# Performance work log

Measured on AMD Instinct MI355X. Metric: run time of the kernel, lower is better.

## Reference

```python
import jax, jax.numpy as jnp
from jax import lax
import numpy as np

D_MODEL = 1024
D_STATE = 128
D_CONV = 4
EXPAND = 2
HEADDIM = 64
CHUNK = 10
D_INNER = EXPAND * D_MODEL          # 2048
NHEADS = D_INNER // HEADDIM         # 32
CONV_DIM = D_INNER + 2 * D_STATE    # 2304
BATCH, SEQ = 2, 1000


def setup_inputs() -> dict:
    key = jax.random.key(0)
    ks = jax.random.split(key, 9)
    n = lambda k, shp, sc: jax.random.normal(k, shp, dtype=jnp.float32) * sc
    return {
        "x": n(ks[0], (BATCH, SEQ, D_MODEL), 1.0),
        "W_in": n(ks[1], (2 * D_INNER + 2 * D_STATE + NHEADS, D_MODEL), 0.02),
        "conv_w": n(ks[2], (CONV_DIM, D_CONV), 0.2),
        "conv_b": n(ks[3], (CONV_DIM,), 0.02),
        "dt_bias": n(ks[4], (NHEADS,), 0.5),
        "A_log": jnp.log(jnp.linspace(1.0, 16.0, NHEADS)).astype(jnp.float32),
        "D": n(ks[6], (NHEADS,), 1.0),
        "norm_w": jnp.ones((D_INNER,), jnp.float32),
        "W_out": n(ks[8], (D_MODEL, D_INNER), 0.02),
    }


def segsum(x):
    # x: (..., T) -> (..., T, T) with out[i,j] = sum_{k=j+1..i} x_k for i>=j else -inf
    cs = jnp.cumsum(x, axis=-1)
    seg = cs[..., :, None] - cs[..., None, :]
    T = x.shape[-1]
    mask = jnp.tril(jnp.ones((T, T), bool))
    return jnp.where(mask, seg, -jnp.inf)


def ssd(x, A, Bm, Cm, chunk):
    # x: (b,l,h,p)  A: (b,l,h)  Bm,Cm: (b,l,n)  (ngroups=1, group dim squeezed)
    b, l, h, p = x.shape
    n = Bm.shape[-1]
    c = l // chunk
    xr = x.reshape(b, c, chunk, h, p)
    Ar = A.reshape(b, c, chunk, h).transpose(0, 3, 1, 2)      # (b,h,c,s)
    Br = Bm.reshape(b, c, chunk, n)
    Cr = Cm.reshape(b, c, chunk, n)
    Acs = jnp.cumsum(Ar, axis=-1)                              # (b,h,c,s)
    L = jnp.exp(segsum(Ar))                                    # (b,h,c,s,s)
    # intra-chunk (diagonal blocks)
    Y_diag = jnp.einsum('bcln,bcsn,bhcls,bcshp->bclhp', Cr, Br, L, xr)
    # per-chunk end states
    decay_states = jnp.exp(Acs[..., -1:] - Acs)                # (b,h,c,s)
    states = jnp.einsum('bcln,bhcl,bclhp->bchpn', Br, decay_states, xr)
    states = jnp.concatenate([jnp.zeros((b, 1, h, p, n), x.dtype), states], axis=1)
    # inter-chunk recurrence (parallel form)
    chunk_sums = jnp.pad(Acs[..., -1], ((0, 0), (0, 0), (1, 0)))  # (b,h,c+1)
    decay_chunk = jnp.exp(segsum(chunk_sums))                    # (b,h,c+1,c+1)
    new_states = jnp.einsum('bhzc,bchpn->bzhpn', decay_chunk, states)
    prev_states = new_states[:, :-1]                             # (b,c,h,p,n)
    # state -> output contribution
    Y_off = jnp.einsum('bcln,bchpn,bhcl->bclhp', Cr, prev_states, jnp.exp(Acs))
    return (Y_diag + Y_off).reshape(b, l, h, p)


def reference(x, W_in, conv_w, conv_b, dt_bias, A_log, D, norm_w, W_out):
    b, l, _ = x.shape
    zxbcdt = x @ W_in.T                                          # (b,l,4384)
    z = zxbcdt[..., :D_INNER]
    xBC = zxbcdt[..., D_INNER:D_INNER + CONV_DIM]
    dt = zxbcdt[..., D_INNER + CONV_DIM:]
    dt = jax.nn.softplus(dt + dt_bias)                           # (b,l,h)
    # causal depthwise conv1d
    xc = jnp.pad(xBC, ((0, 0), (D_CONV - 1, 0), (0, 0)))
    conv = lax.conv_general_dilated(
        xc.transpose(0, 2, 1), conv_w[:, None, :], (1,), 'VALID',
        feature_group_count=CONV_DIM,
        dimension_numbers=('NCH', 'OIH', 'NCH'))
    xBC = jax.nn.silu(conv.transpose(0, 2, 1) + conv_b)          # (b,l,conv_dim)
    x_ssm = xBC[..., :D_INNER].reshape(b, l, NHEADS, HEADDIM)
    Bm = xBC[..., D_INNER:D_INNER + D_STATE]
    Cm = xBC[..., D_INNER + D_STATE:]
    A = -jnp.exp(A_log)                                          # (h,)
    y = ssd(x_ssm * dt[..., None], A * dt, Bm, Cm, CHUNK)
    y = y + x_ssm * D[None, None, :, None]
    y = y.reshape(b, l, D_INNER)
    # gated RMSNorm
    y = y * jax.nn.silu(z)
    y = y * lax.rsqrt(jnp.mean(y * y, axis=-1, keepdims=True) + 1e-5) * norm_w
    return y @ W_out.T
```

## Files before the change

kernel.cpp:

```cpp
#include <hip/hip_runtime.h>
#include <hip/hip_bf16.h>

#define BATCHN 2
#define SEQL 1000
#define DMODEL 1024
#define DSTATE 128
#define HEADDIM 64
#define DINNER 2048
#define NHEADS 32
#define CONVDIM 2304
#define NPROJ 4384
#define TOKENS 2000
#define MPAD 2048
#define NPAD1 4608
#define QC 64
#define NCH 16

typedef __bf16 bfx8 __attribute__((ext_vector_type(8)));
typedef float fx4 __attribute__((ext_vector_type(4)));
typedef unsigned short u16x8 __attribute__((ext_vector_type(8)));

__device__ __forceinline__ unsigned short f2bf(float f) {
    unsigned int u = __builtin_bit_cast(unsigned int, f);
    u += 0x7FFFu + ((u >> 16) & 1u);
    return (unsigned short)(u >> 16);
}
__device__ __forceinline__ float bf2f(unsigned short u) {
    return __builtin_bit_cast(float, ((unsigned int)u) << 16);
}

__device__ __forceinline__ void gload16(const void* g, void* l) {
    __builtin_amdgcn_global_load_lds(
        (const __attribute__((address_space(1))) void*)g,
        (__attribute__((address_space(3))) void*)l, 16, 0, 0);
}

__global__ __launch_bounds__(256) void k_f2bf_pad(const float* __restrict__ src,
                                                  unsigned short* __restrict__ dst,
                                                  int n4src, int n4dst) {
    int i = blockIdx.x * 256 + threadIdx.x;
    if (i >= n4dst) return;
    ushort4 o = {0, 0, 0, 0};
    if (i < n4src) {
        float4 v = ((const float4*)src)[i];
        o.x = f2bf(v.x); o.y = f2bf(v.y); o.z = f2bf(v.z); o.w = f2bf(v.w);
    }
    ((ushort4*)dst)[i] = o;
}

__global__ __launch_bounds__(256) void k_dt(const float* __restrict__ x,
                                            const float* __restrict__ win,
                                            const float* __restrict__ dt_bias,
                                            float* __restrict__ dtv) {
    __shared__ float sx[8][1024];
    int t = threadIdx.x;
    int tok0 = blockIdx.x * 8;
    for (int i = t; i < 8 * 256; i += 256) {
        int tok = i >> 8, k4 = i & 255;
        ((float4*)&sx[tok][0])[k4] = ((const float4*)(x + (size_t)(tok0 + tok) * DMODEL))[k4];
    }
    __syncthreads();
    int tl = t >> 5, h = t & 31;
    const float4* wr_ = (const float4*)(win + (size_t)(2 * DINNER + 2 * DSTATE + h) * DMODEL);
    const float4* xr = (const float4*)&sx[tl][0];
    float acc = 0.f;
    #pragma unroll 4
    for (int k = 0; k < 256; ++k) {
        float4 a = xr[k], b = wr_[k];
        acc += a.x * b.x + a.y * b.y + a.z * b.z + a.w * b.w;
    }
    float v = acc + dt_bias[h];
    dtv[(size_t)(tok0 + tl) * NHEADS + h] = fmaxf(v, 0.f) + log1pf(expf(-fabsf(v)));
}

__global__ __launch_bounds__(512) void k_gemm256(const unsigned short* __restrict__ A,
                                                 const unsigned short* __restrict__ B,
                                                 float* __restrict__ C,
                                                 int Mstore, int N, int K,
                                                 int kc, size_t pstride) {
    __shared__ __attribute__((aligned(16))) unsigned short As[2][4096];
    __shared__ __attribute__((aligned(16))) unsigned short Bs[2][8192];
    int t = threadIdx.x;
    int lane = t & 63, wave = t >> 6;
    int wr = wave >> 2, wc = wave & 3;
    int m0 = blockIdx.y * 128, n0 = blockIdx.x * 256;
    int k0 = blockIdx.z * kc;
    int swcol = (((t & 3) ^ ((t >> 3) & 3)) * 8);
    const unsigned short* Ag  = A + (size_t)(m0 + (t >> 2)) * K + k0 + swcol;
    const unsigned short* Bg0 = B + (size_t)(n0 + (t >> 2)) * K + k0 + swcol;
    const unsigned short* Bg1 = Bg0 + (size_t)128 * K;
    gload16(Ag, &As[0][t * 8]);
    gload16(Bg0, &Bs[0][t * 8]);
    gload16(Bg1, &Bs[0][4096 + t * 8]);
    fx4 acc[4][4] = {};
    int fr = lane & 15, ks = lane >> 4;
    int sl = (ks ^ ((fr >> 1) & 3)) << 3;
    __syncthreads();
    int cur = 0;
    for (int kk = 32; kk < kc; kk += 32) {
        gload16(Ag + kk, &As[cur ^ 1][t * 8]);
        gload16(Bg0 + kk, &Bs[cur ^ 1][t * 8]);
        gload16(Bg1 + kk, &Bs[cur ^ 1][4096 + t * 8]);
        bfx8 a[4], b[4];
        #pragma unroll
        for (int m = 0; m < 4; ++m)
            a[m] = *(const bfx8*)&As[cur][(wr * 64 + m * 16 + fr) * 32 + sl];
        #pragma unroll
        for (int n = 0; n < 4; ++n)
            b[n] = *(const bfx8*)&Bs[cur][(wc * 64 + n * 16 + fr) * 32 + sl];
        #pragma unroll
        for (int m = 0; m < 4; ++m)
            #pragma unroll
            for (int n = 0; n < 4; ++n)
                acc[m][n] = __builtin_amdgcn_mfma_f32_16x16x32_bf16(a[m], b[n], acc[m][n], 0, 0, 0);
        __syncthreads();
        cur ^= 1;
    }
    {
        bfx8 a[4], b[4];
        #pragma unroll
        for (int m = 0; m < 4; ++m)
            a[m] = *(const bfx8*)&As[cur][(wr * 64 + m * 16 + fr) * 32 + sl];
        #pragma unroll
        for (int n = 0; n < 4; ++n)
            b[n] = *(const bfx8*)&Bs[cur][(wc * 64 + n * 16 + fr) * 32 + sl];
        #pragma unroll
        for (int m = 0; m < 4; ++m)
            #pragma unroll
            for (int n = 0; n < 4; ++n)
                acc[m][n] = __builtin_amdgcn_mfma_f32_16x16x32_bf16(a[m], b[n], acc[m][n], 0, 0, 0);
    }
    float* Cz = C + (size_t)blockIdx.z * pstride;
    #pragma unroll
    for (int m = 0; m < 4; ++m) {
        int rbase = m0 + wr * 64 + m * 16 + (lane >> 4) * 4;
        #pragma unroll
        for (int i = 0; i < 4; ++i) {
            int r = rbase + i;
            if (r < Mstore) {
                #pragma unroll
                for (int n = 0; n < 4; ++n) {
                    int c = n0 + wc * 64 + n * 16 + fr;
                    if (c < N) Cz[(size_t)r * N + c] = acc[m][n][i];
                }
            }
        }
    }
}

__global__ __launch_bounds__(256) void k_red(const float* __restrict__ part,
                                             float* __restrict__ out, int n4, size_t pstride4) {
    int i = blockIdx.x * 256 + threadIdx.x;
    if (i >= n4) return;
    const float4* p = (const float4*)part;
    float4 v0 = p[i];
    float4 v1 = p[i + pstride4];
    float4 v2 = p[i + 2 * pstride4];
    float4 v3 = p[i + 3 * pstride4];
    float4 o;
    o.x = (v0.x + v1.x) + (v2.x + v3.x);
    o.y = (v0.y + v1.y) + (v2.y + v3.y);
    o.z = (v0.z + v1.z) + (v2.z + v3.z);
    o.w = (v0.w + v1.w) + (v2.w + v3.w);
    ((float4*)out)[i] = o;
}

__global__ __launch_bounds__(256) void k_conv(const float* __restrict__ zx,
                                              const float* __restrict__ cw,
                                              const float* __restrict__ cb,
                                              float* __restrict__ xbc) {
    int idx = blockIdx.x * 256 + threadIdx.x;
    if (idx >= TOKENS * CONVDIM) return;
    int row = idx / CONVDIM;
    int col = idx - row * CONVDIM;
    int l = row % SEQL;
    float acc = cb[col];
    #pragma unroll
    for (int j = 0; j < 4; ++j) {
        int lj = l - 3 + j;
        if (lj >= 0)
            acc += zx[(size_t)(row - 3 + j) * NPROJ + DINNER + col] * cw[col * 4 + j];
    }
    xbc[idx] = acc / (1.f + expf(-acc));
}

#define SCW 136
#define SWW 72
__global__ __launch_bounds__(256) void k_tile(const float* __restrict__ xbc,
                                              const float* __restrict__ dtv,
                                              const float* __restrict__ A_log,
                                              const float* __restrict__ Dp,
                                              float* __restrict__ ybuf,
                                              float* __restrict__ Sg,
                                              float* __restrict__ cumA) {
    __shared__ unsigned short sC[64 * SCW];
    __shared__ unsigned short sB[64 * SCW];
    __shared__ unsigned short sBdT[128 * SWW];
    __shared__ unsigned short sXdT[64 * SWW];
    __shared__ unsigned short sXr[64 * SWW];
    __shared__ float sAcs[64];
    __shared__ float sdt[64];
    int bid = blockIdx.x;
    int b = bid / (NHEADS * NCH);
    int r = bid % (NHEADS * NCH);
    int h = r / NCH, c = r % NCH;
    int t = threadIdx.x;
    int lane = t & 63, wave = t >> 6;
    if (t < 64) {
        int tok = c * QC + t;
        float d = (tok < SEQL) ? dtv[(size_t)(b * SEQL + tok) * NHEADS + h] : 0.f;
        float A = -expf(A_log[h]);
        float v = A * d;
        #pragma unroll
        for (int off = 1; off < 64; off <<= 1) {
            float u = __shfl_up(v, off, 64);
            if (lane >= off) v += u;
        }
        sdt[t] = d;
        sAcs[t] = v;
        cumA[(size_t)bid * 64 + t] = v;
    }
    __syncthreads();
    float Aend = sAcs[63];
    for (int i = t; i < 64 * 32; i += 256) {
        int l = i >> 5, n4 = (i & 31) * 4;
        int tok = c * QC + l;
        float4 cv = {0, 0, 0, 0}, bv = {0, 0, 0, 0};
        if (tok < SEQL) {
            const float* base = xbc + (size_t)(b * SEQL + tok) * CONVDIM;
            bv = *(const float4*)(base + DINNER + n4);
            cv = *(const float4*)(base + DINNER + DSTATE + n4);
        }
        float dec = expf(Aend - sAcs[l]);
        sC[l * SCW + n4 + 0] = f2bf(cv.x); sC[l * SCW + n4 + 1] = f2bf(cv.y);
        sC[l * SCW + n4 + 2] = f2bf(cv.z); sC[l * SCW + n4 + 3] = f2bf(cv.w);
        sB[l * SCW + n4 + 0] = f2bf(bv.x); sB[l * SCW + n4 + 1] = f2bf(bv.y);
        sB[l * SCW + n4 + 2] = f2bf(bv.z); sB[l * SCW + n4 + 3] = f2bf(bv.w);
        sBdT[(n4 + 0) * SWW + l] = f2bf(bv.x * dec);
        sBdT[(n4 + 1) * SWW + l] = f2bf(bv.y * dec);
        sBdT[(n4 + 2) * SWW + l] = f2bf(bv.z * dec);
        sBdT[(n4 + 3) * SWW + l] = f2bf(bv.w * dec);
    }
    for (int i = t; i < 64 * 16; i += 256) {
        int l = i >> 4, p4 = (i & 15) * 4;
        int tok = c * QC + l;
        float4 xv = {0, 0, 0, 0};
        if (tok < SEQL) xv = *(const float4*)(xbc + (size_t)(b * SEQL + tok) * CONVDIM + h * 64 + p4);
        float d = sdt[l];
        sXr[l * SWW + p4 + 0] = f2bf(xv.x); sXr[l * SWW + p4 + 1] = f2bf(xv.y);
        sXr[l * SWW + p4 + 2] = f2bf(xv.z); sXr[l * SWW + p4 + 3] = f2bf(xv.w);
        sXdT[(p4 + 0) * SWW + l] = f2bf(xv.x * d);
        sXdT[(p4 + 1) * SWW + l] = f2bf(xv.y * d);
        sXdT[(p4 + 2) * SWW + l] = f2bf(xv.z * d);
        sXdT[(p4 + 3) * SWW + l] = f2bf(xv.w * d);
    }
    __syncthreads();
    int fr = lane & 15, fk8 = (lane >> 4) * 8;
    int wr = wave >> 1, wc = wave & 1;
    fx4 g[2][2] = {};
    #pragma unroll
    for (int k = 0; k < 4; ++k) {
        bfx8 a0 = *(const bfx8*)&sC[(wr * 32 + fr) * SCW + k * 32 + fk8];
        bfx8 a1 = *(const bfx8*)&sC[(wr * 32 + 16 + fr) * SCW + k * 32 + fk8];
        bfx8 b0 = *(const bfx8*)&sB[(wc * 32 + fr) * SCW + k * 32 + fk8];
        bfx8 b1 = *(const bfx8*)&sB[(wc * 32 + 16 + fr) * SCW + k * 32 + fk8];
        g[0][0] = __builtin_amdgcn_mfma_f32_16x16x32_bf16(a0, b0, g[0][0], 0, 0, 0);
        g[0][1] = __builtin_amdgcn_mfma_f32_16x16x32_bf16(a0, b1, g[0][1], 0, 0, 0);
        g[1][0] = __builtin_amdgcn_mfma_f32_16x16x32_bf16(a1, b0, g[1][0], 0, 0, 0);
        g[1][1] = __builtin_amdgcn_mfma_f32_16x16x32_bf16(a1, b1, g[1][1], 0, 0, 0);
    }
    __syncthreads();
    int rb = wr * 32 + (lane >> 4) * 4;
    int cb = wc * 32 + fr;
    #pragma unroll
    for (int m = 0; m < 2; ++m)
        #pragma unroll
        for (int n = 0; n < 2; ++n)
            #pragma unroll
            for (int i = 0; i < 4; ++i) {
                int row = rb + m * 16 + i, col = cb + n * 16;
                float wv = (col <= row) ? g[m][n][i] * expf(sAcs[row] - sAcs[col]) : 0.f;
                sB[row * SWW + col] = f2bf(wv);
            }
    __syncthreads();
    fx4 yd[2][2] = {};
    fx4 sc[2][4] = {};
    #pragma unroll
    for (int k = 0; k < 2; ++k) {
        bfx8 aW0 = *(const bfx8*)&sB[(wr * 32 + fr) * SWW + k * 32 + fk8];
        bfx8 aW1 = *(const bfx8*)&sB[(wr * 32 + 16 + fr) * SWW + k * 32 + fk8];
        bfx8 bX0 = *(const bfx8*)&sXdT[(wc * 32 + fr) * SWW + k * 32 + fk8];
        bfx8 bX1 = *(const bfx8*)&sXdT[(wc * 32 + 16 + fr) * SWW + k * 32 + fk8];
        yd[0][0] = __builtin_amdgcn_mfma_f32_16x16x32_bf16(aW0, bX0, yd[0][0], 0, 0, 0);
        yd[0][1] = __builtin_amdgcn_mfma_f32_16x16x32_bf16(aW0, bX1, yd[0][1], 0, 0, 0);
        yd[1][0] = __builtin_amdgcn_mfma_f32_16x16x32_bf16(aW1, bX0, yd[1][0], 0, 0, 0);
        yd[1][1] = __builtin_amdgcn_mfma_f32_16x16x32_bf16(aW1, bX1, yd[1][1], 0, 0, 0);
        bfx8 aX0 = *(const bfx8*)&sXdT[(wr * 32 + fr) * SWW + k * 32 + fk8];
        bfx8 aX1 = *(const bfx8*)&sXdT[(wr * 32 + 16 + fr) * SWW + k * 32 + fk8];
        #pragma unroll
        for (int j = 0; j < 4; ++j) {
            bfx8 bB = *(const bfx8*)&sBdT[(wc * 64 + j * 16 + fr) * SWW + k * 32 + fk8];
            sc[0][j] = __builtin_amdgcn_mfma_f32_16x16x32_bf16(aX0, bB, sc[0][j], 0, 0, 0);
            sc[1][j] = __builtin_amdgcn_mfma_f32_16x16x32_bf16(aX1, bB, sc[1][j], 0, 0, 0);
        }
    }
    float Dh = Dp[h];
    #pragma unroll
    for (int m = 0; m < 2; ++m)
        #pragma unroll
        for (int i = 0; i < 4; ++i) {
            int row = rb + m * 16 + i;
            int tok = c * QC + row;
            if (tok < SEQL) {
                #pragma unroll
                for (int n = 0; n < 2; ++n) {
                    int col = cb + n * 16;
                    float xr = bf2f(sXr[row * SWW + col]);
                    ybuf[(size_t)(b * SEQL + tok) * DINNER + h * 64 + col] = yd[m][n][i] + Dh * xr;
                }
            }
        }
    #pragma unroll
    for (int m = 0; m < 2; ++m)
        #pragma unroll
        for (int i = 0; i < 4; ++i) {
            int p = rb + m * 16 + i;
            #pragma unroll
            for (int j = 0; j < 4; ++j) {
                int n = wc * 64 + j * 16 + fr;
                Sg[(size_t)bid * 8192 + p * 128 + n] = sc[m][j][i];
            }
        }
}

__global__ __launch_bounds__(256) void k_scan2v(float* __restrict__ Sg,
                                                const float* __restrict__ cumA) {
    int bid = blockIdx.x;
    int bh = bid >> 5, sub = bid & 31;
    int e = sub * 256 + threadIdx.x;
    __shared__ float sT[NCH];
    if (threadIdx.x < NCH)
        sT[threadIdx.x] = cumA[((size_t)(bh * NCH) + threadIdx.x) * 64 + 63];
    __syncthreads();
    float S = 0.f;
    size_t base = (size_t)bh * NCH * 8192 + e;
    for (int g = 0; g < NCH; ++g) {
        size_t off = base + (size_t)g * 8192;
        float sg = Sg[off];
        Sg[off] = S;
        S = expf(sT[g]) * S + sg;
    }
}

__global__ __launch_bounds__(256) void k_yoff(const float* __restrict__ xbc,
                                              const float* __restrict__ Sg,
                                              const float* __restrict__ cumA,
                                              float* __restrict__ ybuf) {
    int bid = blockIdx.x;
    int b = bid / (NHEADS * NCH);
    int r = bid % (NHEADS * NCH);
    int h = r / NCH, c = r % NCH;
    if (c == 0) return;
    __shared__ unsigned short sC[64 * SCW];
    __shared__ unsigned short sS[64 * SCW];
    __shared__ float sE[64];
    int t = threadIdx.x;
    int lane = t & 63, wave = t >> 6;
    if (t < 64) sE[t] = expf(cumA[(size_t)bid * 64 + t]);
    for (int i = t; i < 64 * 32; i += 256) {
        int l = i >> 5, n4 = (i & 31) * 4;
        int tok = c * QC + l;
        float4 cv = {0, 0, 0, 0};
        if (tok < SEQL)
            cv = *(const float4*)(xbc + (size_t)(b * SEQL + tok) * CONVDIM + DINNER + DSTATE + n4);
        sC[l * SCW + n4 + 0] = f2bf(cv.x); sC[l * SCW + n4 + 1] = f2bf(cv.y);
        sC[l * SCW + n4 + 2] = f2bf(cv.z); sC[l * SCW + n4 + 3] = f2bf(cv.w);
        float4 sv = *(const float4*)(Sg + (size_t)bid * 8192 + l * 128 + n4);
        sS[l * SCW + n4 + 0] = f2bf(sv.x); sS[l * SCW + n4 + 1] = f2bf(sv.y);
        sS[l * SCW + n4 + 2] = f2bf(sv.z); sS[l * SCW + n4 + 3] = f2bf(sv.w);
    }
    __syncthreads();
    int fr = lane & 15, fk8 = (lane >> 4) * 8;
    int wr = wave >> 1, wc = wave & 1;
    fx4 yo[2][2] = {};
    #pragma unroll
    for (int k = 0; k < 4; ++k) {
        bfx8 a0 = *(const bfx8*)&sC[(wr * 32 + fr) * SCW + k * 32 + fk8];
        bfx8 a1 = *(const bfx8*)&sC[(wr * 32 + 16 + fr) * SCW + k * 32 + fk8];
        bfx8 b0 = *(const bfx8*)&sS[(wc * 32 + fr) * SCW + k * 32 + fk8];
        bfx8 b1 = *(const bfx8*)&sS[(wc * 32 + 16 + fr) * SCW + k * 32 + fk8];
        yo[0][0] = __builtin_amdgcn_mfma_f32_16x16x32_bf16(a0, b0, yo[0][0], 0, 0, 0);
        yo[0][1] = __builtin_amdgcn_mfma_f32_16x16x32_bf16(a0, b1, yo[0][1], 0, 0, 0);
        yo[1][0] = __builtin_amdgcn_mfma_f32_16x16x32_bf16(a1, b0, yo[1][0], 0, 0, 0);
        yo[1][1] = __builtin_amdgcn_mfma_f32_16x16x32_bf16(a1, b1, yo[1][1], 0, 0, 0);
    }
    int rb = wr * 32 + (lane >> 4) * 4;
    int cb = wc * 32 + fr;
    #pragma unroll
    for (int m = 0; m < 2; ++m)
        #pragma unroll
        for (int i = 0; i < 4; ++i) {
            int row = rb + m * 16 + i;
            int tok = c * QC + row;
            if (tok < SEQL) {
                float e = sE[row];
                #pragma unroll
                for (int n = 0; n < 2; ++n) {
                    int col = cb + n * 16;
                    size_t off = (size_t)(b * SEQL + tok) * DINNER + h * 64 + col;
                    ybuf[off] += yo[m][n][i] * e;
                }
            }
        }
}

__global__ __launch_bounds__(256) void k_norm(const float* __restrict__ ybuf,
                                              const float* __restrict__ zx,
                                              const float* __restrict__ normw,
                                              unsigned short* __restrict__ ynb) {
    int row = blockIdx.x;
    int t = threadIdx.x;
    if (row >= TOKENS) {
        #pragma unroll
        for (int j = 0; j < 8; ++j) ynb[(size_t)row * DINNER + t + j * 256] = 0;
        return;
    }
    float v[8];
    float ss = 0.f;
    #pragma unroll
    for (int j = 0; j < 8; ++j) {
        int col = t + j * 256;
        float y = ybuf[(size_t)row * DINNER + col];
        float z = zx[(size_t)row * NPROJ + col];
        y *= z / (1.f + expf(-z));
        v[j] = y;
        ss += y * y;
    }
    #pragma unroll
    for (int off = 32; off > 0; off >>= 1) ss += __shfl_down(ss, off, 64);
    __shared__ float red[4];
    int lane = t & 63, wv = t >> 6;
    if (lane == 0) red[wv] = ss;
    __syncthreads();
    float tot = red[0] + red[1] + red[2] + red[3];
    float r = rsqrtf(tot * (1.f / DINNER) + 1e-5f);
    #pragma unroll
    for (int j = 0; j < 8; ++j) {
        int col = t + j * 256;
        ynb[(size_t)row * DINNER + col] = f2bf(v[j] * r * normw[col]);
    }
}

extern "C" void kernel_launch(void* const* d_in, const int* in_sizes, int n_in,
                              void* d_out, int out_size, void* d_ws, size_t ws_size,
                              hipStream_t stream) {
    const float* x       = (const float*)d_in[0];
    const float* W_in    = (const float*)d_in[1];
    const float* conv_w  = (const float*)d_in[2];
    const float* conv_b  = (const float*)d_in[3];
    const float* dt_bias = (const float*)d_in[4];
    const float* A_log   = (const float*)d_in[5];
    const float* Dp      = (const float*)d_in[6];
    const float* norm_w  = (const float*)d_in[7];
    const float* W_out   = (const float*)d_in[8];
    float* out = (float*)d_out;

    char* w = (char*)d_ws;
    auto alloc = [&](size_t bytes) {
        char* p = w;
        w += (bytes + 255) & ~(size_t)255;
        return p;
    };
    unsigned short* xb    = (unsigned short*)alloc((size_t)MPAD * DMODEL * 2);
    unsigned short* winb  = (unsigned short*)alloc((size_t)NPAD1 * DMODEL * 2);
    unsigned short* woutb = (unsigned short*)alloc((size_t)DMODEL * DINNER * 2);
    float* zx   = (float*)alloc((size_t)TOKENS * NPROJ * 4);
    float* xbc  = (float*)alloc((size_t)TOKENS * CONVDIM * 4);
    float* dtv  = (float*)alloc((size_t)TOKENS * NHEADS * 4);
    float* yb   = (float*)alloc((size_t)TOKENS * DINNER * 4);
    unsigned short* ynb = (unsigned short*)alloc((size_t)MPAD * DINNER * 2);
    float* Sg   = (float*)alloc((size_t)BATCHN * NHEADS * NCH * HEADDIM * DSTATE * 4);
    float* cumA = (float*)alloc((size_t)BATCHN * NHEADS * NCH * 64 * 4);

    int n4;
    n4 = MPAD * DMODEL / 4;
    k_f2bf_pad<<<(n4 + 255) / 256, 256, 0, stream>>>(x, xb, TOKENS * DMODEL / 4, n4);
    n4 = NPAD1 * DMODEL / 4;
    k_f2bf_pad<<<(n4 + 255) / 256, 256, 0, stream>>>(W_in, winb, NPROJ * DMODEL / 4, n4);
    n4 = DMODEL * DINNER / 4;
    k_f2bf_pad<<<(n4 + 255) / 256, 256, 0, stream>>>(W_out, woutb, n4, n4);
    k_dt<<<TOKENS / 8, 256, 0, stream>>>(x, W_in, dt_bias, dtv);
    dim3 g1(NPAD1 / 256, MPAD / 128, 1);
    k_gemm256<<<g1, 512, 0, stream>>>(xb, winb, zx, TOKENS, NPROJ, DMODEL, DMODEL, 0);
    k_conv<<<(TOKENS * CONVDIM + 255) / 256, 256, 0, stream>>>(zx, conv_w, conv_b, xbc);
    k_tile<<<BATCHN * NHEADS * NCH, 256, 0, stream>>>(xbc, dtv, A_log, Dp, yb, Sg, cumA);
    k_scan2v<<<BATCHN * NHEADS * 32, 256, 0, stream>>>(Sg, cumA);
    k_yoff<<<BATCHN * NHEADS * NCH, 256, 0, stream>>>(xbc, Sg, cumA, yb);
    k_norm<<<MPAD, 256, 0, stream>>>(yb, zx, norm_w, ynb);
    size_t pstride = (size_t)MPAD * DMODEL;
    dim3 g2(DMODEL / 256, MPAD / 128, 4);
    k_gemm256<<<g2, 512, 0, stream>>>(ynb, woutb, zx, MPAD, DMODEL, DINNER, DINNER / 4, pstride);
    n4 = TOKENS * DMODEL / 4;
    k_red<<<(n4 + 255) / 256, 256, 0, stream>>>(zx, out, n4, pstride / 4);
}
```

Measured before the change: 193.5 us.

## Fuse prep kernels, shrink GEMM tile to 128x128, register-reuse conv

Merges the three bf16 conversion kernels and the dt projection into a single launch that dispatches on block-index ranges, removing several launches. Replaces the 128x256 GEMM tile with 512 threads by a 128x128 tile with 256 threads and trims W_in padding from 4608 to 4480 rows, so less padded work is done and more blocks are available to fill the CUs. Rewrites the depthwise conv so each thread produces 4 consecutive tokens from 7 loaded inputs, reusing overlapping loads. The smaller tile gives less operand reuse per block in exchange for better occupancy and load balance.

```diff
diff --git a/kernel.cpp b/kernel.cpp
--- a/kernel.cpp
+++ b/kernel.cpp
@@ -12,7 +12,7 @@
 #define NPROJ 4384
 #define TOKENS 2000
 #define MPAD 2048
-#define NPAD1 4608
+#define NPAD1 4480
 #define QC 64
 #define NCH 16
 
@@ -35,72 +35,93 @@
         (__attribute__((address_space(3))) void*)l, 16, 0, 0);
 }
 
-__global__ __launch_bounds__(256) void k_f2bf_pad(const float* __restrict__ src,
-                                                  unsigned short* __restrict__ dst,
-                                                  int n4src, int n4dst) {
-    int i = blockIdx.x * 256 + threadIdx.x;
-    if (i >= n4dst) return;
-    ushort4 o = {0, 0, 0, 0};
-    if (i < n4src) {
-        float4 v = ((const float4*)src)[i];
+#define PB_X   2048
+#define PB_WIN 4480
+#define PB_WO  2048
+#define PB_DT  250
+__global__ __launch_bounds__(256) void k_prep(const float* __restrict__ x,
+                                              const float* __restrict__ win,
+                                              const float* __restrict__ wout,
+                                              const float* __restrict__ dt_bias,
+                                              unsigned short* __restrict__ xb,
+                                              unsigned short* __restrict__ winb,
+                                              unsigned short* __restrict__ woutb,
+                                              float* __restrict__ dtv) {
+    __shared__ float sx[8][1024];
+    int bid = blockIdx.x;
+    int t = threadIdx.x;
+    if (bid < PB_X) {
+        int i = bid * 256 + t;
+        ushort4 o = {0, 0, 0, 0};
+        if (i < TOKENS * DMODEL / 4) {
+            float4 v = ((const float4*)x)[i];
+            o.x = f2bf(v.x); o.y = f2bf(v.y); o.z = f2bf(v.z); o.w = f2bf(v.w);
+        }
+        ((ushort4*)xb)[i] = o;
+    } else if (bid < PB_X + PB_WIN) {
+        int i = (bid - PB_X) * 256 + t;
+        ushort4 o = {0, 0, 0, 0};
+        if (i < NPROJ * DMODEL / 4) {
+            float4 v = ((const float4*)win)[i];
+            o.x = f2bf(v.x); o.y = f2bf(v.y); o.z = f2bf(v.z); o.w = f2bf(v.w);
+        }
+        ((ushort4*)winb)[i] = o;
+    } else if (bid < PB_X + PB_WIN + PB_WO) {
+        int i = (bid - PB_X - PB_WIN) * 256 + t;
+        float4 v = ((const float4*)wout)[i];
+        ushort4 o;
         o.x = f2bf(v.x); o.y = f2bf(v.y); o.z = f2bf(v.z); o.w = f2bf(v.w);
-    }
-    ((ushort4*)dst)[i] = o;
-}
-
-__global__ __launch_bounds__(256) void k_dt(const float* __restrict__ x,
-                                            const float* __restrict__ win,
-                                            const float* __restrict__ dt_bias,
-                                            float* __restrict__ dtv) {
-    __shared__ float sx[8][1024];
-    int t = threadIdx.x;
-    int tok0 = blockIdx.x * 8;
-    for (int i = t; i < 8 * 256; i += 256) {
-        int tok = i >> 8, k4 = i & 255;
-        ((float4*)&sx[tok][0])[k4] = ((const float4*)(x + (size_t)(tok0 + tok) * DMODEL))[k4];
-    }
-    __syncthreads();
-    int tl = t >> 5, h = t & 31;
-    const float4* wr_ = (const float4*)(win + (size_t)(2 * DINNER + 2 * DSTATE + h) * DMODEL);
-    const float4* xr = (const float4*)&sx[tl][0];
-    float acc = 0.f;
-    #pragma unroll 4
-    for (int k = 0; k < 256; ++k) {
-        float4 a = xr[k], b = wr_[k];
-        acc += a.x * b.x + a.y * b.y + a.z * b.z + a.w * b.w;
-    }
-    float v = acc + dt_bias[h];
-    dtv[(size_t)(tok0 + tl) * NHEADS + h] = fmaxf(v, 0.f) + log1pf(expf(-fabsf(v)));
-}
-
-__global__ __launch_bounds__(512) void k_gemm256(const unsigned short* __restrict__ A,
-                                                 const unsigned short* __restrict__ B,
-                                                 float* __restrict__ C,
-                                                 int Mstore, int N, int K,
-                                                 int kc, size_t pstride) {
+        ((ushort4*)woutb)[i] = o;
+    } else {
+        int tok0 = (bid - PB_X - PB_WIN - PB_WO) * 8;
+        for (int i = t; i < 8 * 256; i += 256) {
+            int tok = i >> 8, k4 = i & 255;
+            ((float4*)&sx[tok][0])[k4] = ((const float4*)(x + (size_t)(tok0 + tok) * DMODEL))[k4];
+        }
+        __syncthreads();
+        int tl = t >> 5, h = t & 31;
+        const float4* wr_ = (const float4*)(win + (size_t)(2 * DINNER + 2 * DSTATE + h) * DMODEL);
+        const float4* xr = (const float4*)&sx[tl][0];
+        float acc = 0.f;
+        #pragma unroll 4
+        for (int k = 0; k < 256; ++k) {
+            float4 a = xr[k], b = wr_[k];
+            acc += a.x * b.x + a.y * b.y + a.z * b.z + a.w * b.w;
+        }
+        float v = acc + dt_bias[h];
+        dtv[(size_t)(tok0 + tl) * NHEADS + h] = fmaxf(v, 0.f) + log1pf(expf(-fabsf(v)));
+    }
+}
+
+__global__ __launch_bounds__(256) void k_gemmd(const unsigned short* __restrict__ A,
+                                               const unsigned short* __restrict__ B,
+                                               float* __restrict__ C,
+                                               int Mstore, int N, int K,
+                                               int kc, size_t pstride) {
     __shared__ __attribute__((aligned(16))) unsigned short As[2][4096];
-    __shared__ __attribute__((aligned(16))) unsigned short Bs[2][8192];
+    __shared__ __attribute__((aligned(16))) unsigned short Bs[2][4096];
     int t = threadIdx.x;
     int lane = t & 63, wave = t >> 6;
-    int wr = wave >> 2, wc = wave & 3;
-    int m0 = blockIdx.y * 128, n0 = blockIdx.x * 256;
+    int wr = wave >> 1, wc = wave & 1;
+    int m0 = blockIdx.y * 128, n0 = blockIdx.x * 128;
     int k0 = blockIdx.z * kc;
     int swcol = (((t & 3) ^ ((t >> 3) & 3)) * 8);
-    const unsigned short* Ag  = A + (size_t)(m0 + (t >> 2)) * K + k0 + swcol;
-    const unsigned short* Bg0 = B + (size_t)(n0 + (t >> 2)) * K + k0 + swcol;
-    const unsigned short* Bg1 = Bg0 + (size_t)128 * K;
-    gload16(Ag, &As[0][t * 8]);
-    gload16(Bg0, &Bs[0][t * 8]);
-    gload16(Bg1, &Bs[0][4096 + t * 8]);
-    fx4 acc[4][4] = {};
+    const unsigned short* Ag = A + (size_t)(m0 + (t >> 2)) * K + k0 + swcol;
+    const unsigned short* Bg = B + (size_t)(n0 + (t >> 2)) * K + k0 + swcol;
     int fr = lane & 15, ks = lane >> 4;
     int sl = (ks ^ ((fr >> 1) & 3)) << 3;
+    fx4 acc[4][4] = {};
+    gload16(Ag, &As[0][t * 8]);
+    gload16(Ag + (size_t)64 * K, &As[0][2048 + t * 8]);
+    gload16(Bg, &Bs[0][t * 8]);
+    gload16(Bg + (size_t)64 * K, &Bs[0][2048 + t * 8]);
     __syncthreads();
     int cur = 0;
     for (int kk = 32; kk < kc; kk += 32) {
         gload16(Ag + kk, &As[cur ^ 1][t * 8]);
-        gload16(Bg0 + kk, &Bs[cur ^ 1][t * 8]);
-        gload16(Bg1 + kk, &Bs[cur ^ 1][4096 + t * 8]);
+        gload16(Ag + (size_t)64 * K + kk, &As[cur ^ 1][2048 + t * 8]);
+        gload16(Bg + kk, &Bs[cur ^ 1][t * 8]);
+        gload16(Bg + (size_t)64 * K + kk, &Bs[cur ^ 1][2048 + t * 8]);
         bfx8 a[4], b[4];
         #pragma unroll
         for (int m = 0; m < 4; ++m)
@@ -165,23 +186,29 @@
     ((float4*)out)[i] = o;
 }
 
-__global__ __launch_bounds__(256) void k_conv(const float* __restrict__ zx,
-                                              const float* __restrict__ cw,
-                                              const float* __restrict__ cb,
-                                              float* __restrict__ xbc) {
+__global__ __launch_bounds__(256) void k_conv4(const float* __restrict__ zx,
+                                               const float* __restrict__ cw,
+                                               const float* __restrict__ cb,
+                                               float* __restrict__ xbc) {
     int idx = blockIdx.x * 256 + threadIdx.x;
-    if (idx >= TOKENS * CONVDIM) return;
-    int row = idx / CONVDIM;
-    int col = idx - row * CONVDIM;
-    int l = row % SEQL;
-    float acc = cb[col];
-    #pragma unroll
-    for (int j = 0; j < 4; ++j) {
-        int lj = l - 3 + j;
-        if (lj >= 0)
-            acc += zx[(size_t)(row - 3 + j) * NPROJ + DINNER + col] * cw[col * 4 + j];
-    }
-    xbc[idx] = acc / (1.f + expf(-acc));
+    if (idx >= (TOKENS / 4) * CONVDIM) return;
+    int tg = idx / CONVDIM;
+    int col = idx - tg * CONVDIM;
+    int b = tg / 250;
+    int l0 = (tg - b * 250) * 4;
+    float in[7];
+    #pragma unroll
+    for (int j = 0; j < 7; ++j) {
+        int lj = l0 - 3 + j;
+        in[j] = (lj >= 0) ? zx[(size_t)(b * SEQL + lj) * NPROJ + DINNER + col] : 0.f;
+    }
+    float w0 = cw[col * 4], w1 = cw[col * 4 + 1], w2 = cw[col * 4 + 2], w3 = cw[col * 4 + 3];
+    float bb = cb[col];
+    #pragma unroll
+    for (int i = 0; i < 4; ++i) {
+        float a = bb + w0 * in[i] + w1 * in[i + 1] + w2 * in[i + 2] + w3 * in[i + 3];
+        xbc[(size_t)(b * SEQL + l0 + i) * CONVDIM + col] = a / (1.f + expf(-a));
+    }
 }
 
 #define SCW 136
@@ -482,24 +509,18 @@
     float* Sg   = (float*)alloc((size_t)BATCHN * NHEADS * NCH * HEADDIM * DSTATE * 4);
     float* cumA = (float*)alloc((size_t)BATCHN * NHEADS * NCH * 64 * 4);
 
-    int n4;
-    n4 = MPAD * DMODEL / 4;
-    k_f2bf_pad<<<(n4 + 255) / 256, 256, 0, stream>>>(x, xb, TOKENS * DMODEL / 4, n4);
-    n4 = NPAD1 * DMODEL / 4;
-    k_f2bf_pad<<<(n4 + 255) / 256, 256, 0, stream>>>(W_in, winb, NPROJ * DMODEL / 4, n4);
-    n4 = DMODEL * DINNER / 4;
-    k_f2bf_pad<<<(n4 + 255) / 256, 256, 0, stream>>>(W_out, woutb, n4, n4);
-    k_dt<<<TOKENS / 8, 256, 0, stream>>>(x, W_in, dt_bias, dtv);
-    dim3 g1(NPAD1 / 256, MPAD / 128, 1);
-    k_gemm256<<<g1, 512, 0, stream>>>(xb, winb, zx, TOKENS, NPROJ, DMODEL, DMODEL, 0);
-    k_conv<<<(TOKENS * CONVDIM + 255) / 256, 256, 0, stream>>>(zx, conv_w, conv_b, xbc);
+    k_prep<<<PB_X + PB_WIN + PB_WO + PB_DT, 256, 0, stream>>>(
+        x, W_in, W_out, dt_bias, xb, winb, woutb, dtv);
+    dim3 g1(NPAD1 / 128, MPAD / 128, 1);
+    k_gemmd<<<g1, 256, 0, stream>>>(xb, winb, zx, TOKENS, NPROJ, DMODEL, DMODEL, 0);
+    k_conv4<<<(TOKENS / 4) * CONVDIM / 256, 256, 0, stream>>>(zx, conv_w, conv_b, xbc);
     k_tile<<<BATCHN * NHEADS * NCH, 256, 0, stream>>>(xbc, dtv, A_log, Dp, yb, Sg, cumA);
     k_scan2v<<<BATCHN * NHEADS * 32, 256, 0, stream>>>(Sg, cumA);
     k_yoff<<<BATCHN * NHEADS * NCH, 256, 0, stream>>>(xbc, Sg, cumA, yb);
     k_norm<<<MPAD, 256, 0, stream>>>(yb, zx, norm_w, ynb);
     size_t pstride = (size_t)MPAD * DMODEL;
-    dim3 g2(DMODEL / 256, MPAD / 128, 4);
-    k_gemm256<<<g2, 512, 0, stream>>>(ynb, woutb, zx, MPAD, DMODEL, DINNER, DINNER / 4, pstride);
-    n4 = TOKENS * DMODEL / 4;
+    dim3 g2(DMODEL / 128, MPAD / 128, 4);
+    k_gemmd<<<g2, 256, 0, stream>>>(ynb, woutb, zx, MPAD, DMODEL, DINNER, DINNER / 4, pstride);
+    int n4 = TOKENS * DMODEL / 4;
     k_red<<<(n4 + 255) / 256, 256, 0, stream>>>(zx, out, n4, pstride / 4);
 }
```

After: 260.3 us. +34.5%, slower.
